# Kernel tuning notes

Measured on AMD Instinct MI355X. Metric: run time of the kernel, lower is better.

Reference implementation:

```python
import jax, jax.numpy as jnp
import numpy as np

S, P = 4, 6  # states, stack-encoding depth; detector has S*9**P rows


def _build_cd(s, p):
    """Vectorized construction of ConfigurationDetector1's weight/bias.

    Each of the 9**p multi-indices i = (i_top[0..p-1], i_nonempty[0..p-1]) is
    encoded by p base-9 digits: digit 0 -> (None, None); digit d in 1..8 ->
    symbol v=(d-1)//2 in {0..3} with top present iff (d-1)%2==1.
    convert_to_tensor_indices maps position j (of 2p) value a to column a+4j,
    so i_top occupies cols [0,4p) and i_nonempty cols [4p,8p).
    """
    N9 = 9 ** p
    powers = 9 ** np.arange(p - 1, -1, -1)
    digits = (np.arange(N9)[:, None] // powers) % 9        # (N9, p)
    nonzero = digits > 0
    v = np.where(nonzero, (digits - 1) // 2, 0)            # symbol in {0..3}
    has_top = nonzero & (((digits - 1) % 2) == 1)
    k = nonzero.sum(1) + has_top.sum(1)                    # nnz count per i

    Wi = np.zeros((N9, 8 * p), np.float32)
    rows = np.broadcast_to(np.arange(N9)[:, None], (N9, p))
    col_ne = 4 * p + 4 * np.arange(p) + v                  # nonempty columns
    Wi[rows[nonzero], col_ne[nonzero]] = 1.0
    col_top = 4 * np.arange(p) + v                         # top columns
    Wi[rows[has_top], col_top[has_top]] = 1.0

    R = s * N9                                             # row = i_idx*s + z
    W = np.zeros((R, 8 * p + s), np.float32)
    W[:, :8 * p] = np.repeat(Wi, s, axis=0)
    K = np.repeat(k, s)
    z = np.tile(np.arange(s), N9)
    W[np.arange(R), 8 * p + z] = np.where(K == 0, 1.0, K * (4 * p + 2)).astype(np.float32)
    b = np.where(K == 0, 0.0, -(K * (4 * p + 2)).astype(np.float64)).astype(np.float32)
    return W, b


def _small_linears(p):
    q = 10.0 * p * p
    w_stack = np.zeros((p, 4 * p), np.float32)
    for kk in range(p):
        w_stack[kk, 4 * kk:4 * kk + 4] = 1.0
    w_nss = np.zeros((4 * p, p), np.float32)
    b_nss = np.zeros(4 * p, np.float32)
    w_nst = np.zeros((4 * p, p), np.float32)
    for i in range(p):
        w_nss[4 * i + 0, i] = 1.0
        b_nss[4 * i + 0] = 0.0
        w_nss[4 * i + 1, i] = 1.0 / q
        b_nss[4 * i + 1] = (q - 4 * p - 1) / q
        w_nss[4 * i + 2, i] = 1.0 / q
        b_nss[4 * i + 2] = (q - 1) / q
        w_nss[4 * i + 3, i] = q
        b_nss[4 * i + 3] = -q + 4 * p + 1
        w_nst[4 * i + 3, i] = -4.0
    w_st = ((2 * p + 1) * q * np.eye(4 * p)).astype(np.float32)
    b_st = (-(2 * p + 1) * (q - 2.0) * np.ones(4 * p)).astype(np.float32)
    w_sn = (q * np.eye(4 * p)).astype(np.float32)
    b_sn = (-(q - 4 * p - 2.0) * np.ones(4 * p)).astype(np.float32)
    return w_stack, w_nss, b_nss, w_nst, w_st, b_st, w_sn, b_sn


def setup_inputs() -> dict:
    s, p = S, P
    key = jax.random.key(0)
    kx, kb, kg = jax.random.split(key, 3)
    W, b = _build_cd(s, p)
    R = s * 9 ** p
    bound = 1.0 / np.sqrt(R)  # torch Linear default init bound (fan_in = R)
    beta_w = jax.random.uniform(kb, (s, R), jnp.float32, -bound, bound)
    gamma_w = jax.random.uniform(kg, (4 * p, R), jnp.float32, -bound, bound)
    x = jax.random.normal(kx, (s + 12 * p,), jnp.float32)
    w_stack, w_nss, b_nss, w_nst, w_st, b_st, w_sn, b_sn = _small_linears(p)
    return {
        "x": x,
        "cd_w": jnp.asarray(W), "cd_b": jnp.asarray(b),
        "beta_w": beta_w, "gamma_w": gamma_w,
        "w_stack": jnp.asarray(w_stack),
        "w_nss": jnp.asarray(w_nss), "b_nss": jnp.asarray(b_nss),
        "w_nst": jnp.asarray(w_nst),
        "w_st": jnp.asarray(w_st), "b_st": jnp.asarray(b_st),
        "w_sn": jnp.asarray(w_sn), "b_sn": jnp.asarray(b_sn),
    }


def _sat(v):
    # saturated_relu: sigma(x) = min(max(x, 0), 1)
    return jnp.clip(v, 0.0, 1.0)


def reference(x, cd_w, cd_b, beta_w, gamma_w, w_stack, w_nss, b_nss,
              w_nst, w_st, b_st, w_sn, b_sn):
    s, p = S, P
    state = x[:s]
    noisy_sub_stack = x[s:s + 4 * p]
    noisy_sub_top = x[s + 4 * p:s + 8 * p]
    noisy_sub_nonempty = x[s + 8 * p:]

    w_in = jnp.concatenate([noisy_sub_top, noisy_sub_nonempty, state])  # (8p+s,)
    cd_out = _sat(cd_w @ w_in + cd_b)                                   # (s*9^p,)

    stack = w_stack @ _sat(noisy_sub_stack)                             # (p,)
    top = w_stack @ _sat(noisy_sub_top)                                 # (p,) linear_top is linear_stack

    next_state = beta_w @ cd_out                                        # (s,)
    next_noisy_sub_stack = (w_nss @ stack + b_nss) + (w_nst @ top) + (gamma_w @ cd_out) - 1.0
    next_noisy_sub_top = w_st @ next_noisy_sub_stack + b_st
    next_noisy_sub_nonempty = w_sn @ next_noisy_sub_stack + b_sn
    return jnp.concatenate([next_state, next_noisy_sub_stack,
                            next_noisy_sub_top, next_noisy_sub_nonempty])
```

## Files before the change

### kernel.cpp

```cpp
#include <hip/hip_runtime.h>


#define PN9    531441
#define CHUNKS 64
#define TPB    256

__device__ __forceinline__ float satf(float v) {
    return fminf(fmaxf(v, 0.0f), 1.0f);
}

__global__ __launch_bounds__(TPB) void ss_main(
    const float* __restrict__ x,
    const float* __restrict__ beta_w,
    const float* __restrict__ gamma_w,
    float* __restrict__ partials)
{
    __shared__ float2 tab[54];
    __shared__ float st[4];
    __shared__ float red[TPB / 64];

    const int t = threadIdx.x;
    if (t < 54) {
        const int j = t / 9, d = t % 9;
        float2 e; e.x = 0.0f; e.y = 0.0f;
        if (d > 0) {
            const int v  = (d - 1) >> 1;
            const int ht = (d - 1) & 1;
            e.x = x[52 + 4 * j + v] + (ht ? x[28 + 4 * j + v] : 0.0f);
            e.y = (float)(1 + ht);
        }
        tab[t] = e;
    }
    if (t >= 54 && t < 58) st[t - 54] = x[t - 54];
    __syncthreads();

    const float s0 = st[0], s1 = st[1], s2 = st[2], s3 = st[3];

    const int u = blockIdx.y;
    const float4* __restrict__ row =
        (u < 4) ? ((const float4*)beta_w  + (size_t)u * PN9)
                : ((const float4*)gamma_w + (size_t)(u - 4) * PN9);

    float acc = 0.0f;

    for (int i = blockIdx.x * TPB + t; i < PN9; i += CHUNKS * TPB) {
        unsigned tmp = (unsigned)i;
        float S = 0.0f, K = 0.0f;
#pragma unroll
        for (int j = 5; j >= 0; --j) {
            const unsigned d = tmp % 9u;
            tmp /= 9u;
            const float2 e = tab[j * 9 + d];
            S += e.x;
            K += e.y;
        }
        const float km = 26.0f * K;
        const bool  k0 = (K == 0.0f);
        const float c  = k0 ? 1.0f : km;
        const float base = S - (k0 ? 0.0f : km);

        const float4 v = row[i];
        acc += v.x * satf(base + c * s0)
             + v.y * satf(base + c * s1)
             + v.z * satf(base + c * s2)
             + v.w * satf(base + c * s3);
    }

#pragma unroll
    for (int off = 32; off > 0; off >>= 1) acc += __shfl_down(acc, off, 64);
    const int wave = t >> 6, lane = t & 63;
    if (lane == 0) red[wave] = acc;
    __syncthreads();
    if (t == 0)
        partials[(size_t)u * CHUNKS + blockIdx.x] =
            red[0] + red[1] + red[2] + red[3];
}

__global__ __launch_bounds__(128) void ss_epi(
    const float* __restrict__ x,
    const float* __restrict__ w_stack,
    const float* __restrict__ w_nss, const float* __restrict__ b_nss,
    const float* __restrict__ w_nst,
    const float* __restrict__ w_st,  const float* __restrict__ b_st,
    const float* __restrict__ w_sn,  const float* __restrict__ b_sn,
    const float* __restrict__ partials,
    float* __restrict__ out)
{
    __shared__ float sums[28];
    __shared__ float stk[6], top[6], nns[24];

    const int t = threadIdx.x;

    if (t < 28) {
        float v = 0.0f;
        for (int c = 0; c < CHUNKS; ++c) v += partials[(size_t)t * CHUNKS + c];
        sums[t] = v;
    }
    if (t >= 64 && t < 70) {
        const int k = t - 64;
        float v = 0.0f;
        for (int c = 0; c < 24; ++c) v += w_stack[k * 24 + c] * satf(x[4 + c]);
        stk[k] = v;
    }
    if (t >= 70 && t < 76) {
        const int k = t - 70;
        float v = 0.0f;
        for (int c = 0; c < 24; ++c) v += w_stack[k * 24 + c] * satf(x[28 + c]);
        top[k] = v;
    }
    __syncthreads();

    if (t < 24) {
        float v = b_nss[t] + sums[4 + t] - 1.0f;
        for (int c = 0; c < 6; ++c)
            v += w_nss[t * 6 + c] * stk[c] + w_nst[t * 6 + c] * top[c];
        nns[t] = v;
    }
    __syncthreads();

    if (t < 4) {
        out[t] = sums[t];
    } else if (t < 28) {
        out[t] = nns[t - 4];
    } else if (t < 52) {
        const int r = t - 28;
        float v = b_st[r];
        for (int c = 0; c < 24; ++c) v += w_st[r * 24 + c] * nns[c];
        out[t] = v;
    } else if (t < 76) {
        const int r = t - 52;
        float v = b_sn[r];
        for (int c = 0; c < 24; ++c) v += w_sn[r * 24 + c] * nns[c];
        out[t] = v;
    }
}

extern "C" void kernel_launch(void* const* d_in, const int* in_sizes, int n_in,
                              void* d_out, int out_size, void* d_ws, size_t ws_size,
                              hipStream_t stream) {
    const float* x       = (const float*)d_in[0];
    const float* beta_w  = (const float*)d_in[3];
    const float* gamma_w = (const float*)d_in[4];
    const float* w_stack = (const float*)d_in[5];
    const float* w_nss   = (const float*)d_in[6];
    const float* b_nss   = (const float*)d_in[7];
    const float* w_nst   = (const float*)d_in[8];
    const float* w_st    = (const float*)d_in[9];
    const float* b_st    = (const float*)d_in[10];
    const float* w_sn    = (const float*)d_in[11];
    const float* b_sn    = (const float*)d_in[12];

    float* partials = (float*)d_ws;
    float* out      = (float*)d_out;

    dim3 grid(CHUNKS, 28);
    ss_main<<<grid, TPB, 0, stream>>>(x, beta_w, gamma_w, partials);
    ss_epi<<<1, 128, 0, stream>>>(x, w_stack, w_nss, b_nss, w_nst,
                                  w_st, b_st, w_sn, b_sn, partials, out);
}
```

Before: 46.55 us.

## Pair base-9 digits in lookup table, unroll main loop 4x, parallelize epilogue reduction

```diff
diff --git a/kernel.cpp b/kernel.cpp
--- a/kernel.cpp
+++ b/kernel.cpp
@@ -15,23 +15,30 @@
     const float* __restrict__ gamma_w,
     float* __restrict__ partials)
 {
-    __shared__ float2 tab[54];
+    __shared__ float2 tab2[243];
     __shared__ float st[4];
     __shared__ float red[TPB / 64];
 
     const int t = threadIdx.x;
-    if (t < 54) {
-        const int j = t / 9, d = t % 9;
-        float2 e; e.x = 0.0f; e.y = 0.0f;
-        if (d > 0) {
-            const int v  = (d - 1) >> 1;
-            const int ht = (d - 1) & 1;
-            e.x = x[52 + 4 * j + v] + (ht ? x[28 + 4 * j + v] : 0.0f);
-            e.y = (float)(1 + ht);
+    if (t < 243) {
+        const int jj = t / 81, d2 = t % 81;
+        const int da = d2 / 9;
+        const int db = d2 % 9;
+        float S = 0.0f, K = 0.0f;
+        if (da > 0) {
+            const int v = (da - 1) >> 1, ht = (da - 1) & 1, j = 2 * jj;
+            S += x[52 + 4 * j + v] + (ht ? x[28 + 4 * j + v] : 0.0f);
+            K += (float)(1 + ht);
         }
-        tab[t] = e;
+        if (db > 0) {
+            const int v = (db - 1) >> 1, ht = (db - 1) & 1, j = 2 * jj + 1;
+            S += x[52 + 4 * j + v] + (ht ? x[28 + 4 * j + v] : 0.0f);
+            K += (float)(1 + ht);
+        }
+        float2 e; e.x = S; e.y = K;
+        tab2[t] = e;
     }
-    if (t >= 54 && t < 58) st[t - 54] = x[t - 54];
+    if (t >= 248 && t < 252) st[t - 248] = x[t - 248];
     __syncthreads();
 
     const float s0 = st[0], s1 = st[1], s2 = st[2], s3 = st[3];
@@ -41,16 +48,14 @@
         (u < 4) ? ((const float4*)beta_w  + (size_t)u * PN9)
                 : ((const float4*)gamma_w + (size_t)(u - 4) * PN9);
 
-    float acc = 0.0f;
-
-    for (int i = blockIdx.x * TPB + t; i < PN9; i += CHUNKS * TPB) {
+    auto body = [&](int i, const float4 v) -> float {
         unsigned tmp = (unsigned)i;
         float S = 0.0f, K = 0.0f;
 #pragma unroll
-        for (int j = 5; j >= 0; --j) {
-            const unsigned d = tmp % 9u;
-            tmp /= 9u;
-            const float2 e = tab[j * 9 + d];
+        for (int jj = 2; jj >= 0; --jj) {
+            const unsigned d2 = tmp % 81u;
+            tmp /= 81u;
+            const float2 e = tab2[jj * 81 + d2];
             S += e.x;
             K += e.y;
         }
@@ -58,13 +63,29 @@
         const bool  k0 = (K == 0.0f);
         const float c  = k0 ? 1.0f : km;
         const float base = S - (k0 ? 0.0f : km);
-
-        const float4 v = row[i];
-        acc += v.x * satf(base + c * s0)
+        return v.x * satf(base + c * s0)
              + v.y * satf(base + c * s1)
              + v.z * satf(base + c * s2)
              + v.w * satf(base + c * s3);
+    };
+
+    const int stride = CHUNKS * TPB;
+    float a0 = 0.0f, a1 = 0.0f, a2 = 0.0f, a3 = 0.0f;
+
+    int i = blockIdx.x * TPB + t;
+    for (; i + 3 * stride < PN9; i += 4 * stride) {
+        const float4 v0 = row[i];
+        const float4 v1 = row[i + stride];
+        const float4 v2 = row[i + 2 * stride];
+        const float4 v3 = row[i + 3 * stride];
+        a0 += body(i,              v0);
+        a1 += body(i + stride,     v1);
+        a2 += body(i + 2 * stride, v2);
+        a3 += body(i + 3 * stride, v3);
     }
+    for (; i < PN9; i += stride) a0 += body(i, row[i]);
+
+    float acc = (a0 + a1) + (a2 + a3);
 
 #pragma unroll
     for (int off = 32; off > 0; off >>= 1) acc += __shfl_down(acc, off, 64);
@@ -76,7 +97,7 @@
             red[0] + red[1] + red[2] + red[3];
 }
 
-__global__ __launch_bounds__(128) void ss_epi(
+__global__ __launch_bounds__(256) void ss_epi(
     const float* __restrict__ x,
     const float* __restrict__ w_stack,
     const float* __restrict__ w_nss, const float* __restrict__ b_nss,
@@ -91,19 +112,23 @@
 
     const int t = threadIdx.x;
 
-    if (t < 28) {
+    if (t < 224) {
+        const int u = t >> 3, g = t & 7;
         float v = 0.0f;
-        for (int c = 0; c < CHUNKS; ++c) v += partials[(size_t)t * CHUNKS + c];
-        sums[t] = v;
+#pragma unroll
+        for (int c = 0; c < 8; ++c) v += partials[(size_t)u * CHUNKS + g * 8 + c];
+#pragma unroll
+        for (int off = 4; off > 0; off >>= 1) v += __shfl_down(v, off, 8);
+        if (g == 0) sums[u] = v;
     }
-    if (t >= 64 && t < 70) {
-        const int k = t - 64;
+    if (t >= 224 && t < 230) {
+        const int k = t - 224;
         float v = 0.0f;
         for (int c = 0; c < 24; ++c) v += w_stack[k * 24 + c] * satf(x[4 + c]);
         stk[k] = v;
     }
-    if (t >= 70 && t < 76) {
-        const int k = t - 70;
+    if (t >= 230 && t < 236) {
+        const int k = t - 230;
         float v = 0.0f;
         for (int c = 0; c < 24; ++c) v += w_stack[k * 24 + c] * satf(x[28 + c]);
         top[k] = v;
@@ -155,6 +180,6 @@
 
     dim3 grid(CHUNKS, 28);
     ss_main<<<grid, TPB, 0, stream>>>(x, beta_w, gamma_w, partials);
-    ss_epi<<<1, 128, 0, stream>>>(x, w_stack, w_nss, b_nss, w_nst,
+    ss_epi<<<1, 256, 0, stream>>>(x, w_stack, w_nss, b_nss, w_nst,
                                   w_st, b_st, w_sn, b_sn, partials, out);
 }
```

New measurement: 46.47 us. No clear change (-0.2%).
